# Kernel optimization log

Hardware: AMD Instinct MI355X
Metric: run time of the kernel (lower is better)

Reference implementation:

```python
import jax, jax.numpy as jnp
import numpy as np

LN_EPS = 1e-5  # torch.nn.LayerNorm default


def setup_inputs() -> dict:
    key = jax.random.key(0)
    k1, k2 = jax.random.split(key)
    C = 64
    x = jax.random.normal(k1, (1, C, 64, 96, 96), dtype=jnp.float32)
    ln_gamma = jnp.ones((C,), jnp.float32)
    ln_beta = jnp.zeros((C,), jnp.float32)
    # Conv3d(C, 3C, 1, groups=C) -> per-channel scalar weight [3C] and bias [3C]
    conv_w = jax.random.normal(k2, (3 * C,), dtype=jnp.float32) * 0.02
    conv_b = jnp.zeros((3 * C,), jnp.float32)
    return {"x": x, "ln_gamma": ln_gamma, "ln_beta": ln_beta,
            "conv_w": conv_w, "conv_b": conv_b}


def reference(x, ln_gamma, ln_beta, conv_w, conv_b):
    B, C, D, H, W = x.shape
    N = D * H * W
    xf = x.reshape(B, C, N)  # [B, C, N]

    # LayerNorm over the channel dim (module permutes channels last)
    mean = jnp.mean(xf, axis=1, keepdims=True)
    var = jnp.mean(jnp.square(xf - mean), axis=1, keepdims=True)
    y = (xf - mean) * jax.lax.rsqrt(var + LN_EPS)
    y = y * ln_gamma[None, :, None] + ln_beta[None, :, None]

    # grouped 1x1x1 conv: output channel o reads input channel o // 3
    idx = jnp.arange(3 * C) // 3
    y3 = y[:, idx, :] * conv_w[None, :, None] + conv_b[None, :, None]  # [B, 3C, N]
    q, k, v = jnp.split(y3, 3, axis=1)  # each [B, C, N]

    # channel (cross-covariance) attention: logits [B, C, C]
    logits = jnp.einsum('bcn,bkn->bck', q, k) * (C ** -0.5)
    attn = jax.nn.softmax(logits, axis=-1)  # max-subtraction built in
    out = jnp.einsum('bck,bkn->bcn', attn, v).reshape(B, C, D, H, W)
    return x + out
```

## Files before the change

### kernel.cpp

```cpp
#include <hip/hip_runtime.h>

#define NPOS 589824
#define LN_EPS 1e-5f

typedef _Float16 half8 __attribute__((ext_vector_type(8)));
typedef float f32x4 __attribute__((ext_vector_type(4)));
typedef float f32x2 __attribute__((ext_vector_type(2)));

#define K1_BLOCKS 1152
#define TILE 128
#define CPB 4
#define YSTR 136


__global__ __launch_bounds__(256, 4) void csa_k1(
    const float* __restrict__ x, const float* __restrict__ lng,
    const float* __restrict__ lnb, float* __restrict__ partials)
{
    __shared__ __align__(16) _Float16 Y[45][YSTR];
    __shared__ float SS[256], QQ[256];
    const int tid = threadIdx.x;
    const int lane = tid & 63;
    const int wv = tid >> 6;
    const int p127 = tid & 127;
    const int c0 = (tid >> 7) * 32;

    for (int i = tid; i < YSTR; i += 256) {
        Y[43][i] = (_Float16)1.0f;
        Y[44][i] = (_Float16)0.0f;
    }

    f32x4 acc00 = {0.f,0.f,0.f,0.f}, acc01 = acc00, acc10 = acc00, acc11 = acc00;
    const int row = lane & 15;
    const int sub = (lane >> 4) & 3;
    const int kk = wv * 32 + sub * 8;
    const int r16 = row + 16;
    const int ra1 = (r16 < 22) ? r16 : ((r16 == 22) ? 43 : 44);
    const int rb1 = (r16 < 22) ? (r16 + 21) : ((r16 == 22) ? 43 : 44);
    const int pos0 = blockIdx.x * (CPB * TILE);

    for (int ck = 0; ck < CPB; ++ck) {
        const int n = pos0 + ck * TILE + p127;
        float xv[32];
        #pragma unroll
        for (int i = 0; i < 32; ++i)
            xv[i] = x[(size_t)(c0 + i) * NPOS + n];
        float s = 0.f, sq = 0.f;
        #pragma unroll
        for (int i = 0; i < 32; ++i) { s += xv[i]; sq = fmaf(xv[i], xv[i], sq); }
        SS[tid] = s; QQ[tid] = sq;
        __syncthreads();
        const float st = SS[p127] + SS[p127 + 128];
        const float qt = QQ[p127] + QQ[p127 + 128];
        const float mu  = st * (1.f/64.f);
        const float var = fmaf(-mu, mu, qt * (1.f/64.f));
        const float rin = rsqrtf(fmaxf(var, 0.f) + LN_EPS);
        if (c0 == 0) {
            #pragma unroll
            for (int i = 0; i < 32; ++i)
                Y[i][p127] = (_Float16)fmaf((xv[i] - mu) * rin, lng[i], lnb[i]);
        } else {
            #pragma unroll
            for (int i = 0; i < 11; ++i)
                Y[32 + i][p127] =
                    (_Float16)fmaf((xv[i] - mu) * rin, lng[32 + i], lnb[32 + i]);
        }
        __syncthreads();
        half8 a0 = *(const half8*)&Y[row][kk];
        half8 a1 = *(const half8*)&Y[ra1][kk];
        half8 b0 = *(const half8*)&Y[row + 21][kk];
        half8 b1 = *(const half8*)&Y[rb1][kk];
        acc00 = __builtin_amdgcn_mfma_f32_16x16x32_f16(a0, b0, acc00, 0, 0, 0);
        acc01 = __builtin_amdgcn_mfma_f32_16x16x32_f16(a0, b1, acc01, 0, 0, 0);
        acc10 = __builtin_amdgcn_mfma_f32_16x16x32_f16(a1, b0, acc10, 0, 0, 0);
        acc11 = __builtin_amdgcn_mfma_f32_16x16x32_f16(a1, b1, acc11, 0, 0, 0);
        __syncthreads();
    }

    float* G32 = (float*)&Y[0][0];
    for (int e = tid; e < 1024; e += 256) G32[e] = 0.f;
    __syncthreads();
    const int r0 = (lane >> 4) * 4, cc = lane & 15;
    #pragma unroll
    for (int r = 0; r < 4; ++r) {
        atomicAdd(&G32[(r0 + r) * 32 + cc],            acc00[r]);
        atomicAdd(&G32[(r0 + r) * 32 + 16 + cc],       acc01[r]);
        atomicAdd(&G32[(16 + r0 + r) * 32 + cc],       acc10[r]);
        atomicAdd(&G32[(16 + r0 + r) * 32 + 16 + cc],  acc11[r]);
    }
    __syncthreads();
    for (int e = tid; e < 576; e += 256) {
        const int r = e / 24, c = e % 24;
        partials[(size_t)blockIdx.x * 576 + e] = G32[r * 32 + c];
    }
}

__global__ __launch_bounds__(256) void csa_k2(const float* __restrict__ partials,
                                              float* __restrict__ gfin)
{
    const int tid = threadIdx.x;
    const int e = blockIdx.x * 16 + (tid >> 4);
    const int g = tid & 15;
    float s = 0.f;
    for (int b = g; b < K1_BLOCKS; b += 16)
        s += partials[(size_t)b * 576 + e];
    s += __shfl_down(s, 8, 16);
    s += __shfl_down(s, 4, 16);
    s += __shfl_down(s, 2, 16);
    s += __shfl_down(s, 1, 16);
    if (g == 0) gfin[e] = s;
}

__global__ void csa_k3(const float* __restrict__ G, const float* __restrict__ cw,
                       const float* __restrict__ cb, float* __restrict__ M,
                       float* __restrict__ betaO)
{
    const int c = threadIdx.x;
    __shared__ float lg[64][65];
    const float wq = cw[c], bq = cb[c];
    const int a = c / 3;
    const float Sa = G[a * 24 + 22];
    float mx = -1e30f;
    #pragma unroll
    for (int k = 0; k < 64; ++k) {
        const float wk = cw[64 + k], bk = cb[64 + k];
        const int b = (64 + k) / 3 - 21;
        const float Gab = G[a * 24 + b];
        const float Sb  = G[22 * 24 + b];
        float lo = 0.125f * (wq * wk * Gab + wq * bk * Sa + bq * wk * Sb
                             + bq * bk * (float)NPOS);
        lg[c][k] = lo;
        mx = fmaxf(mx, lo);
    }
    float sum = 0.f;
    #pragma unroll
    for (int k = 0; k < 64; ++k) {
        float e = expf(lg[c][k] - mx);
        lg[c][k] = e; sum += e;
    }
    const float inv = 1.f / sum;
    float Ml[22];
    #pragma unroll
    for (int m = 0; m < 22; ++m) Ml[m] = 0.f;
    float bacc = 0.f;
    #pragma unroll
    for (int k = 0; k < 64; ++k) {
        const float attn = lg[c][k] * inv;
        const int mm = (128 + k) / 3 - 42;
        Ml[mm] = fmaf(attn, cw[128 + k], Ml[mm]);
        bacc   = fmaf(attn, cb[128 + k], bacc);
    }
    #pragma unroll
    for (int m = 0; m < 22; ++m) M[c * 22 + m] = Ml[m];
    betaO[c] = bacc;
}

__global__ __launch_bounds__(256, 2) void csa_k4(
    const float* __restrict__ x, const float* __restrict__ lng,
    const float* __restrict__ lnb, const float* __restrict__ M,
    const float* __restrict__ betaO, float* __restrict__ out)
{
    const int n0 = (blockIdx.x * 256 + threadIdx.x) * 2;
    f32x2 xv[64];
    f32x2 s = {0.f, 0.f}, sq = s;
    #pragma unroll
    for (int c = 0; c < 64; ++c) {
        f32x2 v = *(const f32x2*)(x + (size_t)c * NPOS + n0);
        xv[c] = v; s += v; sq += v * v;
    }
    const f32x2 mu = s * (1.f/64.f);
    const f32x2 var = sq * (1.f/64.f) - mu * mu;
    const float rin0 = rsqrtf(fmaxf(var[0], 0.f) + LN_EPS);
    const float rin1 = rsqrtf(fmaxf(var[1], 0.f) + LN_EPS);
    f32x2 y[22];
    #pragma unroll
    for (int m = 0; m < 22; ++m) {
        const float g = lng[42 + m], b = lnb[42 + m];
        y[m][0] = fmaf((xv[42 + m][0] - mu[0]) * rin0, g, b);
        y[m][1] = fmaf((xv[42 + m][1] - mu[1]) * rin1, g, b);
    }
    #pragma unroll
    for (int c = 0; c < 64; ++c) {
        const float bb = betaO[c];
        f32x2 a = {bb, bb};
        #pragma unroll
        for (int m = 0; m < 22; ++m) {
            const float w = M[c * 22 + m];
            a[0] = fmaf(w, y[m][0], a[0]);
            a[1] = fmaf(w, y[m][1], a[1]);
        }
        f32x2 o = xv[c] + a;
        __builtin_nontemporal_store(o, (f32x2*)(out + (size_t)c * NPOS + n0));
    }
}

extern "C" void kernel_launch(void* const* d_in, const int* in_sizes, int n_in,
                              void* d_out, int out_size, void* d_ws, size_t ws_size,
                              hipStream_t stream) {
    const float* x   = (const float*)d_in[0];
    const float* lng = (const float*)d_in[1];
    const float* lnb = (const float*)d_in[2];
    const float* cw  = (const float*)d_in[3];
    const float* cb  = (const float*)d_in[4];
    float* out = (float*)d_out;

    float* wsf = (float*)d_ws;
    float* Gf  = wsf;
    float* Mf  = wsf + 1024;
    float* Bf  = wsf + 1024 + 64 * 22;
    float* Pf  = (float*)((char*)d_ws + 16384);

    hipLaunchKernelGGL(csa_k1, dim3(K1_BLOCKS), dim3(256), 0, stream,
                       x, lng, lnb, Pf);
    hipLaunchKernelGGL(csa_k2, dim3(36), dim3(256), 0, stream, Pf, Gf);
    hipLaunchKernelGGL(csa_k3, dim3(1), dim3(64), 0, stream, Gf, cw, cb, Mf, Bf);
    hipLaunchKernelGGL(csa_k4, dim3(NPOS / 512), dim3(256), 0, stream,
                       x, lng, lnb, Mf, Bf, out);
}
```

Baseline: 151.3 us.

## Restructure gram kernel to one position per thread with full-channel stats

The gram kernel now assigns one spatial position per thread across all 64 channels, computing LayerNorm stats without shared-memory cross-thread reduction, then re-reads the 43 needed channels (expected to hit in cache) to build the fp16 tile. The block covers 256 positions in one shot instead of looping over four 128-position chunks, which removes the per-chunk barriers. Block count doubles, so there are twice as many partials to write and reduce in the follow-up kernel. Occupancy hint rises to 6 blocks per CU.

```diff
diff --git a/kernel.cpp b/kernel.cpp
--- a/kernel.cpp
+++ b/kernel.cpp
@@ -7,65 +7,54 @@
 typedef float f32x4 __attribute__((ext_vector_type(4)));
 typedef float f32x2 __attribute__((ext_vector_type(2)));
 
-#define K1_BLOCKS 1152
-#define TILE 128
-#define CPB 4
-#define YSTR 136
-
-
-__global__ __launch_bounds__(256, 4) void csa_k1(
+#define GR_BLOCKS 2304
+#define YSTR 264
+
+
+__global__ __launch_bounds__(256, 6) void csa_gram(
     const float* __restrict__ x, const float* __restrict__ lng,
     const float* __restrict__ lnb, float* __restrict__ partials)
 {
     __shared__ __align__(16) _Float16 Y[45][YSTR];
-    __shared__ float SS[256], QQ[256];
     const int tid = threadIdx.x;
     const int lane = tid & 63;
     const int wv = tid >> 6;
-    const int p127 = tid & 127;
-    const int c0 = (tid >> 7) * 32;
+    const int n = blockIdx.x * 256 + tid;
 
     for (int i = tid; i < YSTR; i += 256) {
         Y[43][i] = (_Float16)1.0f;
         Y[44][i] = (_Float16)0.0f;
     }
 
+    float s = 0.f, sq = 0.f;
+    #pragma unroll
+    for (int c = 0; c < 64; ++c) {
+        const float v = x[(size_t)c * NPOS + n];
+        s += v; sq = fmaf(v, v, sq);
+    }
+    const float mu  = s * (1.f/64.f);
+    const float var = fmaf(-mu, mu, sq * (1.f/64.f));
+    const float rin = rsqrtf(fmaxf(var, 0.f) + LN_EPS);
+
+    asm volatile("" ::: "memory");
+
+    #pragma unroll
+    for (int c = 0; c < 43; ++c) {
+        const float v = x[(size_t)c * NPOS + n];
+        Y[c][tid] = (_Float16)fmaf((v - mu) * rin, lng[c], lnb[c]);
+    }
+    __syncthreads();
+
     f32x4 acc00 = {0.f,0.f,0.f,0.f}, acc01 = acc00, acc10 = acc00, acc11 = acc00;
     const int row = lane & 15;
     const int sub = (lane >> 4) & 3;
-    const int kk = wv * 32 + sub * 8;
+    const int kbase = wv * 64 + sub * 8;
     const int r16 = row + 16;
     const int ra1 = (r16 < 22) ? r16 : ((r16 == 22) ? 43 : 44);
     const int rb1 = (r16 < 22) ? (r16 + 21) : ((r16 == 22) ? 43 : 44);
-    const int pos0 = blockIdx.x * (CPB * TILE);
-
-    for (int ck = 0; ck < CPB; ++ck) {
-        const int n = pos0 + ck * TILE + p127;
-        float xv[32];
-        #pragma unroll
-        for (int i = 0; i < 32; ++i)
-            xv[i] = x[(size_t)(c0 + i) * NPOS + n];
-        float s = 0.f, sq = 0.f;
-        #pragma unroll
-        for (int i = 0; i < 32; ++i) { s += xv[i]; sq = fmaf(xv[i], xv[i], sq); }
-        SS[tid] = s; QQ[tid] = sq;
-        __syncthreads();
-        const float st = SS[p127] + SS[p127 + 128];
-        const float qt = QQ[p127] + QQ[p127 + 128];
-        const float mu  = st * (1.f/64.f);
-        const float var = fmaf(-mu, mu, qt * (1.f/64.f));
-        const float rin = rsqrtf(fmaxf(var, 0.f) + LN_EPS);
-        if (c0 == 0) {
-            #pragma unroll
-            for (int i = 0; i < 32; ++i)
-                Y[i][p127] = (_Float16)fmaf((xv[i] - mu) * rin, lng[i], lnb[i]);
-        } else {
-            #pragma unroll
-            for (int i = 0; i < 11; ++i)
-                Y[32 + i][p127] =
-                    (_Float16)fmaf((xv[i] - mu) * rin, lng[32 + i], lnb[32 + i]);
-        }
-        __syncthreads();
+    #pragma unroll
+    for (int s2 = 0; s2 < 2; ++s2) {
+        const int kk = kbase + s2 * 32;
         half8 a0 = *(const half8*)&Y[row][kk];
         half8 a1 = *(const half8*)&Y[ra1][kk];
         half8 b0 = *(const half8*)&Y[row + 21][kk];
@@ -74,8 +63,8 @@
         acc01 = __builtin_amdgcn_mfma_f32_16x16x32_f16(a0, b1, acc01, 0, 0, 0);
         acc10 = __builtin_amdgcn_mfma_f32_16x16x32_f16(a1, b0, acc10, 0, 0, 0);
         acc11 = __builtin_amdgcn_mfma_f32_16x16x32_f16(a1, b1, acc11, 0, 0, 0);
-        __syncthreads();
-    }
+    }
+    __syncthreads();
 
     float* G32 = (float*)&Y[0][0];
     for (int e = tid; e < 1024; e += 256) G32[e] = 0.f;
@@ -102,7 +91,7 @@
     const int e = blockIdx.x * 16 + (tid >> 4);
     const int g = tid & 15;
     float s = 0.f;
-    for (int b = g; b < K1_BLOCKS; b += 16)
+    for (int b = g; b < GR_BLOCKS; b += 16)
         s += partials[(size_t)b * 576 + e];
     s += __shfl_down(s, 8, 16);
     s += __shfl_down(s, 4, 16);
@@ -210,7 +199,7 @@
     float* Bf  = wsf + 1024 + 64 * 22;
     float* Pf  = (float*)((char*)d_ws + 16384);
 
-    hipLaunchKernelGGL(csa_k1, dim3(K1_BLOCKS), dim3(256), 0, stream,
+    hipLaunchKernelGGL(csa_gram, dim3(GR_BLOCKS), dim3(256), 0, stream,
                        x, lng, lnb, Pf);
     hipLaunchKernelGGL(csa_k2, dim3(36), dim3(256), 0, stream, Pf, Gf);
     hipLaunchKernelGGL(csa_k3, dim3(1), dim3(64), 0, stream, Gf, cw, cb, Mf, Bf);
```

Result: slower. 239.5 us (+58.3%).
